# Kernel optimization log

Hardware: AMD Instinct MI355X
Metric: run time of the kernel (lower is better)

## Reference

```python
import jax, jax.numpy as jnp
import numpy as np

N = 50000       # nodes (src == dst set for both blocks)
E = 800000      # edges (avg degree 16)
IN_DIM = 64     # input node feature dim ('attr')
POT_DIM = 16    # potential feature dim ('pot')
H = 64          # h_dim == out_dim == out_edim


def setup_inputs() -> dict:
    key = jax.random.key(0)
    ks = jax.random.split(key, 14)
    g = lambda k, shape, scale: jax.random.normal(k, shape, dtype=jnp.float32) * scale
    return {
        'attr':    g(ks[0], (N, IN_DIM), 1.0),
        'pot0':    g(ks[1], (N, POT_DIM), 1.0),
        'pot1':    g(ks[2], (N, POT_DIM), 1.0),
        'edge_t0': g(ks[3], (E, H), 1.0),
        'edge_t1': g(ks[4], (E, H), 1.0),
        # pot_encoder: Linear(pot_dim, h_dim) + Tanh
        'Wpot': g(ks[5], (POT_DIM, H), POT_DIM ** -0.5),
        'bpot': jnp.zeros((H,), jnp.float32),
        # layer 0: GATLayer(in_dim, h, h, h)
        'fcW0': g(ks[6], (IN_DIM, H), IN_DIM ** -0.5),
        'fcU0': g(ks[7], (IN_DIM, H), IN_DIM ** -0.5),
        'a0':   g(ks[8], (3 * H,), (3 * H) ** -0.5),   # attn_fc weight [z_src|z_dst|t]
        'gate0': jnp.ones((H,), jnp.float32),
        # layer 1: GATLayer(h, h, h, h)
        'fcW1': g(ks[9], (H, H), H ** -0.5),
        'fcU1': g(ks[10], (H, H), H ** -0.5),
        'a1':   g(ks[11], (3 * H,), (3 * H) ** -0.5),
        'gate1': jnp.ones((H,), jnp.float32),
        'src_idx': jax.random.randint(ks[12], (E,), 0, N),
        'dst_idx': jax.random.randint(ks[13], (E,), 0, N),
    }


def _gat_layer(h, v_i, t, src, dst, fcW, fcU, a, gate):
    # h: [N, Din], v_i: [N, H], t: [E, H] (raw edge data 'd'->'t' per original forward)
    Hd = fcW.shape[1]
    z = h @ fcW                 # [N, H] srcdata['z']
    z_i = h @ fcU               # [N, H] dstdata['z_i'] (src set == dst set)
    a_src, a_dst, a_t = a[:Hd], a[Hd:2 * Hd], a[2 * Hd:]
    # attn_fc(cat[z_src, z_dst, t]) decomposed into per-node + per-edge dot products
    score = jax.nn.leaky_relu((z @ a_src)[src] + (z @ a_dst)[dst] + t @ a_t,
                              negative_slope=0.01)        # [E]
    # edge softmax over each dst node's incoming edges
    m = jax.ops.segment_max(score, dst, num_segments=N)   # [N]
    ex = jnp.exp(score - m[dst])                          # [E]
    denom = jax.ops.segment_sum(ex, dst, num_segments=N)  # [N]
    alpha = ex / jnp.where(denom == 0, 1.0, denom)[dst]   # [E]
    z_neighbor = jax.ops.segment_sum(alpha[:, None] * z[src], dst, num_segments=N)
    return z_neighbor + gate * v_i * z_i                  # [N, H]


def reference(attr, pot0, pot1, edge_t0, edge_t1, Wpot, bpot,
              fcW0, fcU0, a0, gate0, fcW1, fcU1, a1, gate1,
              src_idx, dst_idx):
    v0 = jnp.tanh(pot0 @ Wpot + bpot)
    h = _gat_layer(attr, v0, edge_t0, src_idx, dst_idx, fcW0, fcU0, a0, gate0)
    v1 = jnp.tanh(pot1 @ Wpot + bpot)
    h = _gat_layer(h, v1, edge_t1, src_idx, dst_idx, fcW1, fcU1, a1, gate1)
    return h
```

## Files before the change

kernel.cpp:

```cpp
#include <hip/hip_runtime.h>
#include <math.h>

#define NN 50000
#define EE 800000
#define BM 64
#define HB 3125
#define DB 2500
#define DS2 (DB * 256)
#define TB 782

typedef float f4 __attribute__((ext_vector_type(4)));


#define FMA4(acc, s, v) do { \
    (acc).x = fmaf((s), (v).x, (acc).x); \
    (acc).y = fmaf((s), (v).y, (acc).y); \
    (acc).z = fmaf((s), (v).z, (acc).z); \
    (acc).w = fmaf((s), (v).w, (acc).w); } while (0)

__device__ __forceinline__ float dot4(float4 u, float4 v) {
    return fmaf(u.x, v.x, fmaf(u.y, v.y, fmaf(u.z, v.z, u.w * v.w)));
}

__device__ __forceinline__ unsigned pk_bf16(float lo, float hi) {
    union { float f; unsigned u; } a, b;
    a.f = lo; b.f = hi;
    unsigned alo = (a.u + 0x7FFFu + ((a.u >> 16) & 1u)) >> 16;
    unsigned bhi = (b.u + 0x7FFFu + ((b.u >> 16) & 1u)) >> 16;
    return (bhi << 16) | alo;
}

__device__ __forceinline__ float upk_bf16(unsigned u, int odd) {
    union { unsigned u; float f; } r;
    r.u = odd ? (u & 0xFFFF0000u) : (u << 16);
    return r.f;
}


__global__ __launch_bounds__(256) void hist_dot(
    const int* __restrict__ dst, int* __restrict__ deg, int* __restrict__ rank,
    const float* __restrict__ et0, const float* __restrict__ et1,
    const float* __restrict__ a0, const float* __restrict__ a1,
    float* __restrict__ sc0, float* __restrict__ sc1)
{
    const int bid = blockIdx.x;

    if (bid < HB) {
        const int e = bid * 256 + threadIdx.x;
        rank[e] = atomicAdd(&deg[dst[e]], 1);
    } else {
        const int tid  = (bid - HB) * 256 + threadIdx.x;
        const int lane = threadIdx.x & 63;
        const int p    = tid & 15;
        const float4 A0 = *reinterpret_cast<const float4*>(a0 + 128 + p * 4);
        const float4 A1 = *reinterpret_cast<const float4*>(a1 + 128 + p * 4);
        const f4* __restrict__ e0 = reinterpret_cast<const f4*>(et0);
        const f4* __restrict__ e1 = reinterpret_cast<const f4*>(et1);

        for (int i = tid; i < EE * 16; i += DS2 * 4) {
            f4 v0[4], v1[4];
#pragma unroll
            for (int u = 0; u < 4; u++) v0[u] = __builtin_nontemporal_load(e0 + i + u * DS2);
#pragma unroll
            for (int u = 0; u < 4; u++) v1[u] = __builtin_nontemporal_load(e1 + i + u * DS2);
            float r0[4], r1[4];
#pragma unroll
            for (int u = 0; u < 4; u++) {
                r0[u] = fmaf(v0[u][0], A0.x, fmaf(v0[u][1], A0.y, fmaf(v0[u][2], A0.z, v0[u][3] * A0.w)));
                r1[u] = fmaf(v1[u][0], A1.x, fmaf(v1[u][1], A1.y, fmaf(v1[u][2], A1.z, v1[u][3] * A1.w)));
            }
#pragma unroll
            for (int u = 0; u < 4; u++) {
#pragma unroll
                for (int off = 8; off; off >>= 1) {
                    r0[u] += __shfl_xor(r0[u], off);
                    r1[u] += __shfl_xor(r1[u], off);
                }
            }
            if ((lane & 15) == 0) {
#pragma unroll
                for (int u = 0; u < 4; u++) {
                    const int e = (i + u * DS2) >> 4;
                    sc0[e] = r0[u];
                    sc1[e] = r1[u];
                }
            }
        }
    }
}


__global__ __launch_bounds__(256) void k_scatter(
    const int* __restrict__ src, const int* __restrict__ dst,
    const int* __restrict__ rowptr, const int* __restrict__ rank,
    const float* __restrict__ sc0, const float* __restrict__ sc1,
    int2* __restrict__ epA, int2* __restrict__ epB)
{
    int e = blockIdx.x * 256 + threadIdx.x;
    if (e < EE) {
        const int p = rowptr[dst[e]] + rank[e];
        const int s = src[e];
        epA[p] = make_int2(s, __float_as_int(sc0[e]));
        epB[p] = make_int2(s, __float_as_int(sc1[e]));
    }
}


__global__ __launch_bounds__(256) void node_transform(
    const float* __restrict__ hin, const float* __restrict__ pot,
    const float* __restrict__ Wpot, const float* __restrict__ bpot,
    const float* __restrict__ fcW, const float* __restrict__ fcU,
    const float* __restrict__ a, const float* __restrict__ gate,
    unsigned* __restrict__ zb, float* __restrict__ zs, float* __restrict__ zd,
    float* __restrict__ base,
    const int* __restrict__ deg, int* __restrict__ rowptr, int do_scan)
{
    __shared__ float sAt[64][64];
    __shared__ float sB[64][128];
    __shared__ float sPot[64][16];
    __shared__ float sWp[16][64];

    const int t = threadIdx.x;

    if (do_scan && blockIdx.x == TB) {
        int* part = reinterpret_cast<int*>(&sAt[0][0]);
        const int CH = (NN + 255) / 256;
        const int b  = t * CH;
        const int e  = min(b + CH, NN);
        int sum = 0;
        for (int i = b; i < e; i++) sum += deg[i];
        part[t] = sum;
        __syncthreads();
        for (int off = 1; off < 256; off <<= 1) {
            int v = (t >= off) ? part[t - off] : 0;
            __syncthreads();
            part[t] += v;
            __syncthreads();
        }
        int run = (t == 0) ? 0 : part[t - 1];
        for (int i = b; i < e; i++) {
            rowptr[i] = run;
            run += deg[i];
        }
        if (t == 0) rowptr[NN] = EE;
        return;
    }

    const int m0    = blockIdx.x * BM;
    const int valid = min(BM, NN - m0);

#pragma unroll
    for (int j = 0; j < 4; j++) {
        const int idx = t + j * 256;
        const int kw = idx >> 4, cq = idx & 15;
        *reinterpret_cast<float4*>(&sB[kw][cq * 4]) =
            *reinterpret_cast<const float4*>(fcW + kw * 64 + cq * 4);
        *reinterpret_cast<float4*>(&sB[kw][64 + cq * 4]) =
            *reinterpret_cast<const float4*>(fcU + kw * 64 + cq * 4);
    }
    {
        const int m = t >> 2, q = t & 3;
#pragma unroll
        for (int i = 0; i < 4; i++) {
            const int kg = i * 4 + q;
            float4 v4 = make_float4(0.f, 0.f, 0.f, 0.f);
            if (m < valid)
                v4 = *reinterpret_cast<const float4*>(hin + (size_t)(m0 + m) * 64 + kg * 4);
            sAt[kg * 4 + 0][m] = v4.x;
            sAt[kg * 4 + 1][m] = v4.y;
            sAt[kg * 4 + 2][m] = v4.z;
            sAt[kg * 4 + 3][m] = v4.w;
        }
        float4 p4 = make_float4(0.f, 0.f, 0.f, 0.f);
        if (m < valid)
            p4 = *reinterpret_cast<const float4*>(pot + (size_t)(m0 + m) * 16 + q * 4);
        *reinterpret_cast<float4*>(&sPot[m][q * 4]) = p4;
    }
    {
        const int kk = t >> 4, cq = t & 15;
        *reinterpret_cast<float4*>(&sWp[kk][cq * 4]) =
            *reinterpret_cast<const float4*>(Wpot + kk * 64 + cq * 4);
    }
    __syncthreads();

    const int c4 = (t & 15) * 4;
    const int r4 = (t >> 4) * 4;

    float4 az[4], au[4];
#pragma unroll
    for (int i = 0; i < 4; i++) {
        az[i] = make_float4(0.f, 0.f, 0.f, 0.f);
        au[i] = make_float4(0.f, 0.f, 0.f, 0.f);
    }

#pragma unroll 4
    for (int k = 0; k < 64; k++) {
        const float4 a4 = *reinterpret_cast<const float4*>(&sAt[k][r4]);
        const float4 bw = *reinterpret_cast<const float4*>(&sB[k][c4]);
        const float4 bu = *reinterpret_cast<const float4*>(&sB[k][64 + c4]);
        FMA4(az[0], a4.x, bw); FMA4(au[0], a4.x, bu);
        FMA4(az[1], a4.y, bw); FMA4(au[1], a4.y, bu);
        FMA4(az[2], a4.z, bw); FMA4(au[2], a4.z, bu);
        FMA4(az[3], a4.w, bw); FMA4(au[3], a4.w, bu);
    }

    {
        const float4 as4 = *reinterpret_cast<const float4*>(a + c4);
        const float4 ad4 = *reinterpret_cast<const float4*>(a + 64 + c4);
        float ps[4], pd[4];
#pragma unroll
        for (int i = 0; i < 4; i++) { ps[i] = dot4(az[i], as4); pd[i] = dot4(az[i], ad4); }
#pragma unroll
        for (int off = 1; off < 16; off <<= 1) {
#pragma unroll
            for (int i = 0; i < 4; i++) {
                ps[i] += __shfl_xor(ps[i], off);
                pd[i] += __shfl_xor(pd[i], off);
            }
        }
        if ((t & 15) == 0) {
#pragma unroll
            for (int i = 0; i < 4; i++) {
                if (r4 + i < valid) {
                    zs[m0 + r4 + i] = ps[i];
                    zd[m0 + r4 + i] = pd[i];
                }
            }
        }
    }

    {
        const float4 bp4 = *reinterpret_cast<const float4*>(bpot + c4);
        const float4 g4  = *reinterpret_cast<const float4*>(gate + c4);
        float4 vv[4] = {bp4, bp4, bp4, bp4};
#pragma unroll
        for (int kk = 0; kk < 16; kk++) {
            const float4 wp = *reinterpret_cast<const float4*>(&sWp[kk][c4]);
#pragma unroll
            for (int i = 0; i < 4; i++) {
                const float pv = sPot[r4 + i][kk];
                FMA4(vv[i], pv, wp);
            }
        }
#pragma unroll
        for (int i = 0; i < 4; i++) {
            if (r4 + i < valid) {
                const int n = m0 + r4 + i;
                uint2 zp;
                zp.x = pk_bf16(az[i].x, az[i].y);
                zp.y = pk_bf16(az[i].z, az[i].w);
                *reinterpret_cast<uint2*>(zb + (size_t)n * 32 + c4 / 2) = zp;
                float4 b;
                b.x = g4.x * tanhf(vv[i].x) * au[i].x;
                b.y = g4.y * tanhf(vv[i].y) * au[i].y;
                b.z = g4.z * tanhf(vv[i].z) * au[i].z;
                b.w = g4.w * tanhf(vv[i].w) * au[i].w;
                *reinterpret_cast<float4*>(base + (size_t)n * 64 + c4) = b;
            }
        }
    }
}


__global__ __launch_bounds__(256) void node_sm_agg(
    const int* __restrict__ rowptr, const int2* __restrict__ ep,
    const float* __restrict__ zs, const float* __restrict__ zd,
    const unsigned* __restrict__ zb, const float* __restrict__ base,
    float* __restrict__ out)
{
    const int lane = threadIdx.x & 63;
    const int n    = blockIdx.x * 4 + (threadIdx.x >> 6);
    if (n >= NN) return;

    const int s0  = rowptr[n], s1 = rowptr[n + 1];
    const int deg = s1 - s0;
    const float zdn = zd[n];
    const int half = lane >> 1;
    const int odd  = lane & 1;

    float acc = 0.f;
    float ds;

    if (deg <= 64) {
        const int j = s0 + lane;
        int   sv = 0;
        float sc = -INFINITY;
        if (j < s1) {
            const int2 pr = ep[j];
            sv = pr.x;
            float v = __int_as_float(pr.y) + zs[sv] + zdn;
            sc = (v >= 0.f) ? v : 0.01f * v;
        }
        float mx = sc;
#pragma unroll
        for (int off = 32; off; off >>= 1) mx = fmaxf(mx, __shfl_xor(mx, off));
        float ex = (j < s1) ? __expf(sc - mx) : 0.f;
        ds = ex;
#pragma unroll
        for (int off = 32; off; off >>= 1) ds += __shfl_xor(ds, off);

        int t = 0;
        for (; t + 8 <= deg; t += 8) {
            int   ss[8]; float ee[8]; unsigned uu[8];
#pragma unroll
            for (int u = 0; u < 8; u++) {
                ss[u] = __shfl(sv, t + u);
                ee[u] = __shfl(ex, t + u);
            }
#pragma unroll
            for (int u = 0; u < 8; u++) uu[u] = zb[(size_t)ss[u] * 32 + half];
#pragma unroll
            for (int u = 0; u < 8; u++) acc = fmaf(ee[u], upk_bf16(uu[u], odd), acc);
        }
        for (; t + 4 <= deg; t += 4) {
            int   ss[4]; float ee[4]; unsigned uu[4];
#pragma unroll
            for (int u = 0; u < 4; u++) {
                ss[u] = __shfl(sv, t + u);
                ee[u] = __shfl(ex, t + u);
            }
#pragma unroll
            for (int u = 0; u < 4; u++) uu[u] = zb[(size_t)ss[u] * 32 + half];
#pragma unroll
            for (int u = 0; u < 4; u++) acc = fmaf(ee[u], upk_bf16(uu[u], odd), acc);
        }
        for (; t < deg; t++) {
            int   s = __shfl(sv, t);
            float e = __shfl(ex, t);
            acc = fmaf(e, upk_bf16(zb[(size_t)s * 32 + half], odd), acc);
        }
    } else {
        float mx = -INFINITY;
        for (int j = s0 + lane; j < s1; j += 64) {
            const int2 pr = ep[j];
            float v = __int_as_float(pr.y) + zs[pr.x] + zdn;
            v = (v >= 0.f) ? v : 0.01f * v;
            mx = fmaxf(mx, v);
        }
#pragma unroll
        for (int off = 32; off; off >>= 1) mx = fmaxf(mx, __shfl_xor(mx, off));
        ds = 0.f;
        for (int c0 = s0; c0 < s1; c0 += 64) {
            const int j = c0 + lane;
            int   sv = 0;
            float ex = 0.f;
            if (j < s1) {
                const int2 pr = ep[j];
                sv = pr.x;
                float v = __int_as_float(pr.y) + zs[sv] + zdn;
                v = (v >= 0.f) ? v : 0.01f * v;
                ex = __expf(v - mx);
            }
            ds += ex;
            const int cnt = min(64, s1 - c0);
            for (int t = 0; t < cnt; t++) {
                int   s = __shfl(sv, t);
                float e = __shfl(ex, t);
                acc = fmaf(e, upk_bf16(zb[(size_t)s * 32 + half], odd), acc);
            }
        }
#pragma unroll
        for (int off = 32; off; off >>= 1) ds += __shfl_xor(ds, off);
    }

    float r = 1.f / ((ds == 0.f) ? 1.f : ds);
    const size_t o = (size_t)n * 64 + lane;
    out[o] = acc * r + base[o];
}


extern "C" void kernel_launch(void* const* d_in, const int* in_sizes, int n_in,
                              void* d_out, int out_size, void* d_ws, size_t ws_size,
                              hipStream_t stream)
{
    const float* attr  = (const float*)d_in[0];
    const float* pot0  = (const float*)d_in[1];
    const float* pot1  = (const float*)d_in[2];
    const float* et0   = (const float*)d_in[3];
    const float* et1   = (const float*)d_in[4];
    const float* Wpot  = (const float*)d_in[5];
    const float* bpot  = (const float*)d_in[6];
    const float* fcW0  = (const float*)d_in[7];
    const float* fcU0  = (const float*)d_in[8];
    const float* a0    = (const float*)d_in[9];
    const float* gate0 = (const float*)d_in[10];
    const float* fcW1  = (const float*)d_in[11];
    const float* fcU1  = (const float*)d_in[12];
    const float* a1    = (const float*)d_in[13];
    const float* gate1 = (const float*)d_in[14];
    const int*   src   = (const int*)d_in[15];
    const int*   dst   = (const int*)d_in[16];

    float* out = (float*)d_out;

    int2*     epA    = (int2*)d_ws;
    int2*     epB    = epA + EE;
    unsigned* zb     = (unsigned*)(epB + EE);
    float*    base   = (float*)(zb + NN * 32);
    float*    zs     = base + NN * 64;
    float*    zd     = zs + NN;
    float*    sc0    = zd + NN;
    float*    sc1    = sc0 + EE;
    int*      rowptr = (int*)(sc1 + EE);
    int*      deg    = rowptr + NN + 1;
    int*      rank   = deg + NN;

    const int eblk = (EE + 255) / 256;
    const int nblk = (NN + 3) / 4;

    hipMemsetAsync(deg, 0, NN * sizeof(int), stream);

    hist_dot<<<HB + DB, 256, 0, stream>>>(dst, deg, rank, et0, et1, a0, a1, sc0, sc1);

    node_transform<<<TB + 1, 256, 0, stream>>>(attr, pot0, Wpot, bpot, fcW0, fcU0,
                                               a0, gate0, zb, zs, zd, base,
                                               deg, rowptr, 1);

    k_scatter<<<eblk, 256, 0, stream>>>(src, dst, rowptr, rank, sc0, sc1, epA, epB);

    node_sm_agg<<<nblk, 256, 0, stream>>>(rowptr, epA, zs, zd, zb, base, out);

    node_transform<<<TB, 256, 0, stream>>>(out, pot1, Wpot, bpot, fcW1, fcU1,
                                           a1, gate1, zb, zs, zd, base,
                                           deg, rowptr, 0);
    node_sm_agg<<<nblk, 256, 0, stream>>>(rowptr, epB, zs, zd, zb, base, out);
}
```

Measured before the change: 330.7 us.

## Process two nodes per wavefront in softmax-aggregation, drop nontemporal edge loads

The edge-softmax aggregation kernel now gives each node a 32-lane half-wavefront instead of a full 64-lane wavefront. Each lane unpacks both bf16 values of a packed word and writes a float2, so one wave handles two nodes. The small-degree fast path now covers degrees up to 32, and the loop runs to the larger degree of the two halves. This is meant to halve the per-edge lane work and the shuffle and reduction cost at the average degree of 16. Separately, the edge-feature dot kernel switches from nontemporal loads to ordinary loads. If the two halves of a wave take different degree branches, the cross-half degree exchange may read an inactive lane.

Result: slower. 359.6 us (+8.8%).

```diff
diff --git a/kernel.cpp b/kernel.cpp
--- a/kernel.cpp
+++ b/kernel.cpp
@@ -28,12 +28,6 @@
     unsigned alo = (a.u + 0x7FFFu + ((a.u >> 16) & 1u)) >> 16;
     unsigned bhi = (b.u + 0x7FFFu + ((b.u >> 16) & 1u)) >> 16;
     return (bhi << 16) | alo;
-}
-
-__device__ __forceinline__ float upk_bf16(unsigned u, int odd) {
-    union { unsigned u; float f; } r;
-    r.u = odd ? (u & 0xFFFF0000u) : (u << 16);
-    return r.f;
 }
 
 
@@ -60,9 +54,9 @@
         for (int i = tid; i < EE * 16; i += DS2 * 4) {
             f4 v0[4], v1[4];
 #pragma unroll
-            for (int u = 0; u < 4; u++) v0[u] = __builtin_nontemporal_load(e0 + i + u * DS2);
-#pragma unroll
-            for (int u = 0; u < 4; u++) v1[u] = __builtin_nontemporal_load(e1 + i + u * DS2);
+            for (int u = 0; u < 4; u++) v0[u] = e0[i + u * DS2];
+#pragma unroll
+            for (int u = 0; u < 4; u++) v1[u] = e1[i + u * DS2];
             float r0[4], r1[4];
 #pragma unroll
             for (int u = 0; u < 4; u++) {
@@ -269,20 +263,21 @@
     float* __restrict__ out)
 {
     const int lane = threadIdx.x & 63;
-    const int n    = blockIdx.x * 4 + (threadIdx.x >> 6);
+    const int half = lane >> 5;
+    const int sl   = lane & 31;
+    const int hb   = half << 5;
+    const int n    = blockIdx.x * 8 + ((threadIdx.x >> 6) << 1) + half;
     if (n >= NN) return;
 
     const int s0  = rowptr[n], s1 = rowptr[n + 1];
     const int deg = s1 - s0;
     const float zdn = zd[n];
-    const int half = lane >> 1;
-    const int odd  = lane & 1;
-
-    float acc = 0.f;
+
+    float2 acc = make_float2(0.f, 0.f);
     float ds;
 
-    if (deg <= 64) {
-        const int j = s0 + lane;
+    if (deg <= 32) {
+        const int j = s0 + sl;
         int   sv = 0;
         float sc = -INFINITY;
         if (j < s1) {
@@ -293,55 +288,53 @@
         }
         float mx = sc;
 #pragma unroll
-        for (int off = 32; off; off >>= 1) mx = fmaxf(mx, __shfl_xor(mx, off));
+        for (int off = 16; off; off >>= 1) mx = fmaxf(mx, __shfl_xor(mx, off));
         float ex = (j < s1) ? __expf(sc - mx) : 0.f;
         ds = ex;
 #pragma unroll
-        for (int off = 32; off; off >>= 1) ds += __shfl_xor(ds, off);
+        for (int off = 16; off; off >>= 1) ds += __shfl_xor(ds, off);
+
+        int mdeg = deg;
+        mdeg = max(mdeg, __shfl_xor(mdeg, 32));
 
         int t = 0;
-        for (; t + 8 <= deg; t += 8) {
-            int   ss[8]; float ee[8]; unsigned uu[8];
+        for (; t + 8 <= mdeg; t += 8) {
+            int ss[8]; float ee[8]; unsigned uu[8];
 #pragma unroll
             for (int u = 0; u < 8; u++) {
-                ss[u] = __shfl(sv, t + u);
-                ee[u] = __shfl(ex, t + u);
-            }
-#pragma unroll
-            for (int u = 0; u < 8; u++) uu[u] = zb[(size_t)ss[u] * 32 + half];
-#pragma unroll
-            for (int u = 0; u < 8; u++) acc = fmaf(ee[u], upk_bf16(uu[u], odd), acc);
-        }
-        for (; t + 4 <= deg; t += 4) {
-            int   ss[4]; float ee[4]; unsigned uu[4];
-#pragma unroll
-            for (int u = 0; u < 4; u++) {
-                ss[u] = __shfl(sv, t + u);
-                ee[u] = __shfl(ex, t + u);
-            }
-#pragma unroll
-            for (int u = 0; u < 4; u++) uu[u] = zb[(size_t)ss[u] * 32 + half];
-#pragma unroll
-            for (int u = 0; u < 4; u++) acc = fmaf(ee[u], upk_bf16(uu[u], odd), acc);
-        }
-        for (; t < deg; t++) {
-            int   s = __shfl(sv, t);
-            float e = __shfl(ex, t);
-            acc = fmaf(e, upk_bf16(zb[(size_t)s * 32 + half], odd), acc);
+                ss[u] = __shfl(sv, hb + t + u);
+                ee[u] = __shfl(ex, hb + t + u);
+            }
+#pragma unroll
+            for (int u = 0; u < 8; u++) uu[u] = zb[(size_t)ss[u] * 32 + sl];
+#pragma unroll
+            for (int u = 0; u < 8; u++) {
+                const float zl = __uint_as_float(uu[u] << 16);
+                const float zh = __uint_as_float(uu[u] & 0xFFFF0000u);
+                acc.x = fmaf(ee[u], zl, acc.x);
+                acc.y = fmaf(ee[u], zh, acc.y);
+            }
+        }
+        for (; t < mdeg; t++) {
+            const int   s = __shfl(sv, hb + t);
+            const float e = __shfl(ex, hb + t);
+            const unsigned u = zb[(size_t)s * 32 + sl];
+            acc.x = fmaf(e, __uint_as_float(u << 16), acc.x);
+            acc.y = fmaf(e, __uint_as_float(u & 0xFFFF0000u), acc.y);
         }
     } else {
         float mx = -INFINITY;
-        for (int j = s0 + lane; j < s1; j += 64) {
+        for (int j = s0 + sl; j < s1; j += 32) {
             const int2 pr = ep[j];
             float v = __int_as_float(pr.y) + zs[pr.x] + zdn;
             v = (v >= 0.f) ? v : 0.01f * v;
             mx = fmaxf(mx, v);
         }
 #pragma unroll
-        for (int off = 32; off; off >>= 1) mx = fmaxf(mx, __shfl_xor(mx, off));
+        for (int off = 16; off; off >>= 1) mx = fmaxf(mx, __shfl_xor(mx, off));
         ds = 0.f;
-        for (int c0 = s0; c0 < s1; c0 += 64) {
-            const int j = c0 + lane;
+        for (int c0 = s0; c0 < s1; c0 += 32) {
+            const int j = c0 + sl;
             int   sv = 0;
             float ex = 0.f;
             if (j < s1) {
@@ -352,20 +345,26 @@
                 ex = __expf(v - mx);
             }
             ds += ex;
-            const int cnt = min(64, s1 - c0);
+            const int cnt = min(32, s1 - c0);
             for (int t = 0; t < cnt; t++) {
-                int   s = __shfl(sv, t);
-                float e = __shfl(ex, t);
-                acc = fmaf(e, upk_bf16(zb[(size_t)s * 32 + half], odd), acc);
-            }
-        }
-#pragma unroll
-        for (int off = 32; off; off >>= 1) ds += __shfl_xor(ds, off);
-    }
-
-    float r = 1.f / ((ds == 0.f) ? 1.f : ds);
-    const size_t o = (size_t)n * 64 + lane;
-    out[o] = acc * r + base[o];
+                const int   s = __shfl(sv, hb + t);
+                const float e = __shfl(ex, hb + t);
+                const unsigned u = zb[(size_t)s * 32 + sl];
+                acc.x = fmaf(e, __uint_as_float(u << 16), acc.x);
+                acc.y = fmaf(e, __uint_as_float(u & 0xFFFF0000u), acc.y);
+            }
+        }
+#pragma unroll
+        for (int off = 16; off; off >>= 1) ds += __shfl_xor(ds, off);
+    }
+
+    const float r = 1.f / ((ds == 0.f) ? 1.f : ds);
+    const size_t o = (size_t)n * 64 + sl * 2;
+    const float2 b2 = *reinterpret_cast<const float2*>(base + o);
+    float2 res;
+    res.x = acc.x * r + b2.x;
+    res.y = acc.y * r + b2.y;
+    *reinterpret_cast<float2*>(out + o) = res;
 }
 
 
@@ -405,8 +404,8 @@
     int*      deg    = rowptr + NN + 1;
     int*      rank   = deg + NN;
 
-    const int eblk = (EE + 255) / 256;
-    const int nblk = (NN + 3) / 4;
+    const int eblk  = (EE + 255) / 256;
+    const int nblk2 = (NN + 7) / 8;
 
     hipMemsetAsync(deg, 0, NN * sizeof(int), stream);
 
@@ -418,10 +417,10 @@
 
     k_scatter<<<eblk, 256, 0, stream>>>(src, dst, rowptr, rank, sc0, sc1, epA, epB);
 
-    node_sm_agg<<<nblk, 256, 0, stream>>>(rowptr, epA, zs, zd, zb, base, out);
+    node_sm_agg<<<nblk2, 256, 0, stream>>>(rowptr, epA, zs, zd, zb, base, out);
 
     node_transform<<<TB, 256, 0, stream>>>(out, pot1, Wpot, bpot, fcW1, fcU1,
                                            a1, gate1, zb, zs, zd, base,
                                            deg, rowptr, 0);
-    node_sm_agg<<<nblk, 256, 0, stream>>>(rowptr, epB, zs, zd, zb, base, out);
-}
+    node_sm_agg<<<nblk2, 256, 0, stream>>>(rowptr, epB, zs, zd, zb, base, out);
+}
```
